# Optimization experiments

Hardware: AMD Instinct MI355X
Metric: run time of the kernel (lower is better)

## Reference

```python
import jax, jax.numpy as jnp
import numpy as np

N_NODES = 100000


def gcn_conv(x, edge_index, W, b):
    # PyG GCNConv: add self-loops, symmetric normalization D^-1/2 (A+I) D^-1/2, transform, aggregate, bias.
    src, dst = edge_index[0], edge_index[1]
    n = x.shape[0]
    xw = x @ W  # [N, out] transform before propagate (PyG order)
    # degree with self-loops (count edges by target + 1)
    deg = jax.ops.segment_sum(jnp.ones_like(dst, dtype=xw.dtype), dst, num_segments=n) + 1.0
    dinv = jax.lax.rsqrt(deg)  # deg >= 1, safe
    norm = dinv[src] * dinv[dst]  # [E]
    msgs = xw[src] * norm[:, None]  # [E, out] gathered, normalized messages
    agg = jax.ops.segment_sum(msgs, dst, num_segments=n)
    # self-loop contribution: norm_ii = dinv_i^2 = 1/deg_i
    agg = agg + xw * (dinv * dinv)[:, None]
    return agg + b


def setup_inputs() -> dict:
    key = jax.random.key(0)
    ks = jax.random.split(key, 8)
    in_c, h1, h2, out_c = 128, 71, 82, 1
    x = jax.random.normal(ks[0], (N_NODES, in_c), dtype=jnp.float32)
    edge_index = jax.random.randint(ks[1], (2, 1600000), 0, N_NODES, dtype=jnp.int64)
    def glorot(k, fan_in, fan_out):
        s = jnp.sqrt(6.0 / (fan_in + fan_out))
        return jax.random.uniform(k, (fan_in, fan_out), jnp.float32, -s, s)
    return {
        "x": x,
        "edge_index": edge_index,
        "W1": glorot(ks[2], in_c, h1), "b1": jnp.zeros((h1,), jnp.float32),
        "W2": glorot(ks[3], h1, h2), "b2": jnp.zeros((h2,), jnp.float32),
        "W3": glorot(ks[4], h2, out_c), "b3": jnp.zeros((out_c,), jnp.float32),
    }


def reference(x, edge_index, W1, b1, W2, b2, W3, b3):
    h = jax.nn.relu(gcn_conv(x, edge_index, W1, b1))
    h = gcn_conv(h, edge_index, W2, b2)  # note: no relu after conv2 in source
    return gcn_conv(h, edge_index, W3, b3)
```

## Files before the change

### kernel.cpp

```cpp
#include <hip/hip_runtime.h>
#include <hip/hip_fp16.h>

#define NNODES 100000
#define NB 196
#define BSHIFT 9
#define BMASK 511
#define BCAP 9216
#define WT_LD 136

typedef _Float16 half8 __attribute__((ext_vector_type(8)));
typedef float floatx4 __attribute__((ext_vector_type(4)));

__global__ void binA_kernel(const int* __restrict__ src, const int* __restrict__ dst,
                            int* __restrict__ bcnt, unsigned* __restrict__ bdata, int E) {
    __shared__ int hist[NB];
    __shared__ int gb[NB];
    __shared__ int cur[NB];
    const int BATCH = 4096;
    for (int base = blockIdx.x * BATCH; base < E; base += gridDim.x * BATCH) {
        for (int i = threadIdx.x; i < NB; i += blockDim.x) hist[i] = 0;
        __syncthreads();
        int s[16], d[16];
        int cnt = 0;
        if (base + BATCH <= E) {
#pragma unroll
            for (int q = 0; q < 4; ++q) {
                int4 sv = ((const int4*)(src + base))[q * 256 + threadIdx.x];
                int4 dv = ((const int4*)(dst + base))[q * 256 + threadIdx.x];
                s[cnt] = sv.x; d[cnt] = dv.x; atomicAdd(&hist[dv.x >> BSHIFT], 1); ++cnt;
                s[cnt] = sv.y; d[cnt] = dv.y; atomicAdd(&hist[dv.y >> BSHIFT], 1); ++cnt;
                s[cnt] = sv.z; d[cnt] = dv.z; atomicAdd(&hist[dv.z >> BSHIFT], 1); ++cnt;
                s[cnt] = sv.w; d[cnt] = dv.w; atomicAdd(&hist[dv.w >> BSHIFT], 1); ++cnt;
            }
        } else {
#pragma unroll
            for (int k = 0; k < 16; ++k) {
                int idx = base + k * 256 + threadIdx.x;
                if (idx < E) {
                    s[cnt] = src[idx];
                    d[cnt] = dst[idx];
                    atomicAdd(&hist[d[cnt] >> BSHIFT], 1);
                    ++cnt;
                }
            }
        }
        __syncthreads();
        for (int i = threadIdx.x; i < NB; i += blockDim.x) {
            int c = hist[i];
            gb[i] = (c > 0) ? atomicAdd(&bcnt[i], c) : 0;
            cur[i] = 0;
        }
        __syncthreads();
        for (int k = 0; k < cnt; ++k) {
            int b = d[k] >> BSHIFT;
            int lo = gb[b] + atomicAdd(&cur[b], 1);
            if (lo < BCAP)
                bdata[(size_t)b * BCAP + lo] = ((unsigned)s[k] << BSHIFT) | ((unsigned)d[k] & BMASK);
        }
        __syncthreads();
    }
}

__global__ __launch_bounds__(1024) void prep_kernel(
        const int* __restrict__ bcnt, int* __restrict__ bstart,
        const float* __restrict__ W2, const float* __restrict__ b2,
        const float* __restrict__ W3, float* __restrict__ w23,
        const float* __restrict__ W1, __half* __restrict__ Wt) {
    if (blockIdx.x == 0) {
        __shared__ int sh[NB];
        int t = threadIdx.x;
        if (t < NB) sh[t] = min(bcnt[t], BCAP);
        __syncthreads();
        if (t == 0) {
            int acc = 0;
            for (int i = 0; i < NB; ++i) { int v = sh[i]; sh[i] = acc; acc += v; }
        }
        __syncthreads();
        if (t < NB) bstart[t] = sh[t];
    } else if (blockIdx.x == 1) {
        int k = threadIdx.x;
        if (k < 71) {
            float a = 0.f;
            for (int j = 0; j < 82; ++j) a += W2[k * 82 + j] * W3[j];
            w23[k] = a;
        } else if (k == 71) {
            float a = 0.f;
            for (int j = 0; j < 82; ++j) a += b2[j] * W3[j];
            w23[71] = a;
        }
    } else {
        for (int i = threadIdx.x; i < 80 * WT_LD; i += blockDim.x) {
            int nn = i / WT_LD, k = i - nn * WT_LD;
            float v = (nn < 71 && k < 128) ? W1[k * 71 + nn] : 0.f;
            Wt[i] = __float2half(v);
        }
    }
}

__global__ __launch_bounds__(1024) void binB2_kernel(
        const int* __restrict__ bcnt, const int* __restrict__ bstart,
        const unsigned* __restrict__ bdata,
        int* __restrict__ deg, int* __restrict__ end_off, float* __restrict__ dinv,
        int* __restrict__ csr, int n) {
    __shared__ unsigned edata[BCAP];
    __shared__ int hist[512];
    __shared__ int cur[512];
    __shared__ int wsum[8];
    int b = blockIdx.x;
    int tid = threadIdx.x;
    int cnt = min(bcnt[b], BCAP);
    int base = bstart[b];
    const unsigned* p = bdata + (size_t)b * BCAP;
    if (tid < 512) hist[tid] = 0;
    __syncthreads();
    for (int i = tid; i < cnt; i += 1024) {
        unsigned e = p[i];
        edata[i] = e;
        atomicAdd(&hist[e & BMASK], 1);
    }
    __syncthreads();
    if (tid < 512) {
        int v = hist[tid];
        int lane = tid & 63;
        int incl = v;
#pragma unroll
        for (int off = 1; off < 64; off <<= 1) {
            int t = __shfl_up(incl, off);
            if (lane >= off) incl += t;
        }
        cur[tid] = incl;
        if (lane == 63) wsum[tid >> 6] = incl;
    }
    __syncthreads();
    if (tid == 0) {
        int acc = 0;
#pragma unroll
        for (int w = 0; w < 8; ++w) { int t = wsum[w]; wsum[w] = acc; acc += t; }
    }
    __syncthreads();
    if (tid < 512) {
        int v = hist[tid];
        int start = base + wsum[tid >> 6] + cur[tid] - v;
        int node = (b << BSHIFT) + tid;
        if (node < n) {
            deg[node] = v;
            end_off[node] = start + v;
            dinv[node] = rsqrtf((float)v + 1.0f);
        }
        cur[tid] = start;
    }
    __syncthreads();
    for (int i = tid; i < cnt; i += 1024) {
        unsigned e = edata[i];
        int pos = atomicAdd(&cur[e & BMASK], 1);
        csr[pos] = (int)(e >> BSHIFT);
    }
}

__global__ __launch_bounds__(256) void xform_mfma(
        const float* __restrict__ x, const __half* __restrict__ Wt,
        const float* __restrict__ scale, __half* __restrict__ msgA,
        __half* __restrict__ msgB, int n) {
    __shared__ __half Wsh[80 * WT_LD];
    {
        const uint4* sp = (const uint4*)Wt;
        uint4* dp = (uint4*)Wsh;
        for (int i = threadIdx.x; i < (80 * WT_LD * 2) / 16; i += blockDim.x) dp[i] = sp[i];
    }
    __syncthreads();
    int lane = threadIdx.x & 63;
    int m = lane & 15, q = lane >> 4;
    int gw = (blockIdx.x * blockDim.x + threadIdx.x) >> 6;
    int nw = (gridDim.x * blockDim.x) >> 6;
    int nrt = n >> 4;
    for (int rt = gw; rt < nrt; rt += nw) {
        int rb = rt << 4;
        const float* xr = x + (size_t)(rb + m) * 128 + q * 8;
        floatx4 acc[5];
#pragma unroll
        for (int t = 0; t < 5; ++t) acc[t] = (floatx4){0.f, 0.f, 0.f, 0.f};
#pragma unroll
        for (int ks = 0; ks < 4; ++ks) {
            float4 f0 = *(const float4*)(xr + ks * 32);
            float4 f1 = *(const float4*)(xr + ks * 32 + 4);
            half8 a;
            a[0] = (_Float16)f0.x; a[1] = (_Float16)f0.y;
            a[2] = (_Float16)f0.z; a[3] = (_Float16)f0.w;
            a[4] = (_Float16)f1.x; a[5] = (_Float16)f1.y;
            a[6] = (_Float16)f1.z; a[7] = (_Float16)f1.w;
#pragma unroll
            for (int t = 0; t < 5; ++t) {
                half8 b = *(const half8*)&Wsh[(t * 16 + m) * WT_LD + ks * 32 + q * 8];
                acc[t] = __builtin_amdgcn_mfma_f32_16x16x32_f16(a, b, acc[t], 0, 0, 0);
            }
        }
        float sc[4];
#pragma unroll
        for (int r = 0; r < 4; ++r) sc[r] = scale[rb + q * 4 + r];
#pragma unroll
        for (int t = 0; t < 5; ++t) {
            int col = t * 16 + m;
#pragma unroll
            for (int r = 0; r < 4; ++r) {
                __half hv = __float2half(acc[t][r] * sc[r]);
                int row = rb + q * 4 + r;
                if (t < 4) {
                    msgA[(size_t)row * 64 + col] = hv;
                } else if (m < 8) {
                    msgB[(size_t)row * 8 + m] = hv;
                }
            }
        }
    }
}

__global__ __launch_bounds__(256) void gather_fused(
        const __half2* __restrict__ msgA, const __half2* __restrict__ msgB,
        const int* __restrict__ csr, const int* __restrict__ end_off,
        const int* __restrict__ deg, const float* __restrict__ dinv,
        const float* __restrict__ b, const float* __restrict__ w23,
        float* __restrict__ g2, int n) {
    int lane = threadIdx.x & 63;
    int wid = (blockIdx.x * blockDim.x + threadIdx.x) >> 6;
    int nwaves = (gridDim.x * blockDim.x) >> 6;
    int k = lane & 31;
    int c = k << 1;
    float bxA = b[c], byA = b[c + 1];
    float w0A = w23[c], w1A = w23[c + 1];
    int p = lane & 3;
    int cb = 64 + (p << 1);
    float bxB = b[cb];
    float byB = (cb + 1 < 71) ? b[cb + 1] : 0.f;
    float w0B = w23[cb];
    float w1B = (cb + 1 < 71) ? w23[cb + 1] : 0.f;
    const char* mA = (const char*)msgA;
    const char* mB = (const char*)msgB;
    unsigned laneOffA = (unsigned)(k << 2);
    unsigned laneOffB = (unsigned)(p << 2);
    for (int node = wid; node < n; node += nwaves) {
        int end = end_off[node];
        int cnt = deg[node];
        int start = end - cnt;
        float ax0 = 0.f, ay0 = 0.f, ax1 = 0.f, ay1 = 0.f;
        float ax2 = 0.f, ay2 = 0.f, ax3 = 0.f, ay3 = 0.f;
        float bxs = 0.f, bys = 0.f;
        for (int base = 0; base < cnt; base += 64) {
            int rem = min(cnt - base, 64);
            int se = (lane < rem) ? csr[start + base + lane] : 0;
            int j = 0;
            for (; j + 7 < rem; j += 8) {
                int sa0 = __builtin_amdgcn_readlane(se, j + 0);
                int sb0 = __builtin_amdgcn_readlane(se, j + 1);
                int sa1 = __builtin_amdgcn_readlane(se, j + 2);
                int sb1 = __builtin_amdgcn_readlane(se, j + 3);
                int sa2 = __builtin_amdgcn_readlane(se, j + 4);
                int sb2 = __builtin_amdgcn_readlane(se, j + 5);
                int sa3 = __builtin_amdgcn_readlane(se, j + 6);
                int sb3 = __builtin_amdgcn_readlane(se, j + 7);
                int s0 = (lane < 32) ? sa0 : sb0;
                int s1 = (lane < 32) ? sa1 : sb1;
                int s2 = (lane < 32) ? sa2 : sb2;
                int s3 = (lane < 32) ? sa3 : sb3;
                float2 v0 = __half22float2(*(const __half2*)(mA + (((unsigned)s0 << 7) | laneOffA)));
                float2 v1 = __half22float2(*(const __half2*)(mA + (((unsigned)s1 << 7) | laneOffA)));
                float2 v2 = __half22float2(*(const __half2*)(mA + (((unsigned)s2 << 7) | laneOffA)));
                float2 v3 = __half22float2(*(const __half2*)(mA + (((unsigned)s3 << 7) | laneOffA)));
                ax0 += v0.x; ay0 += v0.y;  ax1 += v1.x; ay1 += v1.y;
                ax2 += v2.x; ay2 += v2.y;  ax3 += v3.x; ay3 += v3.y;
            }
            for (; j + 1 < rem; j += 2) {
                int sa = __builtin_amdgcn_readlane(se, j);
                int sb = __builtin_amdgcn_readlane(se, j + 1);
                int s = (lane < 32) ? sa : sb;
                float2 v = __half22float2(*(const __half2*)(mA + (((unsigned)s << 7) | laneOffA)));
                ax0 += v.x; ay0 += v.y;
            }
            if (j < rem) {
                int s = __builtin_amdgcn_readlane(se, j);
                float2 v = __half22float2(*(const __half2*)(mA + (((unsigned)s << 7) | laneOffA)));
                if (lane < 32) { ax0 += v.x; ay0 += v.y; }
            }
            for (int t = 0; t < rem; t += 16) {
                int idx = t + (lane >> 2);
                int ss = __shfl(se, (idx < rem) ? idx : (rem - 1));
                float2 v = __half22float2(*(const __half2*)(mB + (((unsigned)ss << 4) | laneOffB)));
                if (idx < rem) { bxs += v.x; bys += v.y; }
            }
        }
        float axA = (ax0 + ax1) + (ax2 + ax3);
        float ayA = (ay0 + ay1) + (ay2 + ay3);
        axA += __shfl_xor(axA, 32);
        ayA += __shfl_xor(ayA, 32);
        {
            float2 sv = __half22float2(msgA[(size_t)node * 32 + k]);
            axA += sv.x; ayA += sv.y;
        }
        bxs += __shfl_xor(bxs, 4);  bxs += __shfl_xor(bxs, 8);
        bxs += __shfl_xor(bxs, 16); bxs += __shfl_xor(bxs, 32);
        bys += __shfl_xor(bys, 4);  bys += __shfl_xor(bys, 8);
        bys += __shfl_xor(bys, 16); bys += __shfl_xor(bys, 32);
        {
            float2 sv = __half22float2(msgB[(size_t)node * 4 + p]);
            bxs += sv.x; bys += sv.y;
        }
        float dv = dinv[node];
        float pa = fmaxf(dv * axA + bxA, 0.f) * w0A + fmaxf(dv * ayA + byA, 0.f) * w1A;
        float pb = fmaxf(dv * bxs + bxB, 0.f) * w0B + fmaxf(dv * bys + byB, 0.f) * w1B;
        float r = ((lane < 32) ? pa : 0.f) + ((lane < 4) ? pb : 0.f);
#pragma unroll
        for (int off = 32; off > 0; off >>= 1) r += __shfl_down(r, off);
        if (lane == 0) g2[node] = dv * r;
    }
}

__global__ void sgather_q(const float* __restrict__ g2, const int* __restrict__ csr,
                          const int* __restrict__ end_off, const int* __restrict__ deg,
                          const float* __restrict__ dinv, const float* __restrict__ w23,
                          float* __restrict__ q, int n) {
    float bw = w23[71];
    int lane = threadIdx.x & 63;
    int g = lane >> 4, k = lane & 15;
    int wid = (blockIdx.x * blockDim.x + threadIdx.x) >> 6;
    int nw = (gridDim.x * blockDim.x) >> 6;
    for (int i0 = wid * 4; i0 < n; i0 += nw * 4) {
        int i = i0 + g;
        float acc = 0.f;
        float dv = 0.f;
        if (i < n) {
            int end = end_off[i];
            int cnt = deg[i];
            int start = end - cnt;
            dv = dinv[i];
            for (int e = k; e < cnt; e += 16) acc += g2[csr[start + e]];
        }
        acc += __shfl_down(acc, 8, 16);
        acc += __shfl_down(acc, 4, 16);
        acc += __shfl_down(acc, 2, 16);
        acc += __shfl_down(acc, 1, 16);
        if (i < n && k == 0) q[i] = dv * (dv * (acc + g2[i]) + bw);
    }
}

__global__ void sgather_out(const float* __restrict__ q, const int* __restrict__ csr,
                            const int* __restrict__ end_off, const int* __restrict__ deg,
                            const float* __restrict__ dinv, const float* __restrict__ b3,
                            float* __restrict__ out, int n) {
    float bv = b3[0];
    int lane = threadIdx.x & 63;
    int g = lane >> 4, k = lane & 15;
    int wid = (blockIdx.x * blockDim.x + threadIdx.x) >> 6;
    int nw = (gridDim.x * blockDim.x) >> 6;
    for (int i0 = wid * 4; i0 < n; i0 += nw * 4) {
        int i = i0 + g;
        float acc = 0.f;
        float dv = 0.f;
        if (i < n) {
            int end = end_off[i];
            int cnt = deg[i];
            int start = end - cnt;
            dv = dinv[i];
            for (int e = k; e < cnt; e += 16) acc += q[csr[start + e]];
        }
        acc += __shfl_down(acc, 8, 16);
        acc += __shfl_down(acc, 4, 16);
        acc += __shfl_down(acc, 2, 16);
        acc += __shfl_down(acc, 1, 16);
        if (i < n && k == 0) out[i] = dv * (acc + q[i]) + bv;
    }
}

extern "C" void kernel_launch(void* const* d_in, const int* in_sizes, int n_in,
                              void* d_out, int out_size, void* d_ws, size_t ws_size,
                              hipStream_t stream) {
    const float* x  = (const float*)d_in[0];
    const int*   ei = (const int*)d_in[1];
    const float* W1 = (const float*)d_in[2];
    const float* b1 = (const float*)d_in[3];
    const float* W2 = (const float*)d_in[4];
    const float* b2 = (const float*)d_in[5];
    const float* W3 = (const float*)d_in[6];
    const float* b3 = (const float*)d_in[7];
    float* out = (float*)d_out;

    const int n = NNODES;
    const int E = in_sizes[1] / 2;
    const int* src = ei;
    const int* dst = ei + E;

    float* ws     = (float*)d_ws;
    float* dinv   = ws;
    int*   deg_i  = (int*)(ws + n);
    int*   offs   = deg_i + n;
    int*   bcnt   = offs + n;
    int*   bstart = bcnt + 256;
    float* w23    = (float*)(bstart + 256);
    __half* Wt    = (__half*)(w23 + 80);
    float* g2     = (float*)(Wt + 11008);
    float* q      = g2 + n;
    int*   csr    = (int*)(q + n);
    __half* msgA  = (__half*)(csr + E + 16);
    __half* msgB  = msgA + (size_t)n * 64;
    unsigned* bdata = (unsigned*)(msgB + (size_t)n * 8);

    hipMemsetAsync(bcnt, 0, 256 * sizeof(int), stream);
    binA_kernel<<<(E + 4095) / 4096, 256, 0, stream>>>(src, dst, bcnt, bdata, E);
    prep_kernel<<<3, 1024, 0, stream>>>(bcnt, bstart, W2, b2, W3, w23, W1, Wt);
    binB2_kernel<<<NB, 1024, 0, stream>>>(bcnt, bstart, bdata, deg_i, offs, dinv, csr, n);

    xform_mfma<<<1563, 256, 0, stream>>>(x, Wt, dinv, msgA, msgB, n);

    gather_fused<<<2048, 256, 0, stream>>>((const __half2*)msgA, (const __half2*)msgB,
                                           csr, offs, deg_i, dinv, b1, w23, g2, n);

    sgather_q<<<1024, 256, 0, stream>>>(g2, csr, offs, deg_i, dinv, w23, q, n);
    sgather_out<<<1024, 256, 0, stream>>>(q, csr, offs, deg_i, dinv, b3, out, n);
}
```

Measured before the change: 238.9 us.

## Gather eight nodes per wavefront with 16-byte half8 row loads

Restructures the first-layer gather so each wavefront handles a tile of 8 nodes, 8 lanes per node. Each lane loads a 16-byte half8 slice of the 64-wide message row plus one half of the tail columns, replacing the one-node-per-wave scheme with 4-byte loads and readlane broadcasts. CSR indices are prefetched two steps ahead, and the self-loop is folded into the loop as an extra iteration. The aim is better memory-level parallelism and fewer idle lanes on low-degree nodes. In exchange, all 8 nodes in a tile iterate to the tile's maximum degree, which leaves lanes idle when degrees vary.

```diff
diff --git a/kernel.cpp b/kernel.cpp
--- a/kernel.cpp
+++ b/kernel.cpp
@@ -215,101 +215,82 @@
 }
 
 __global__ __launch_bounds__(256) void gather_fused(
-        const __half2* __restrict__ msgA, const __half2* __restrict__ msgB,
+        const __half* __restrict__ msgA, const __half* __restrict__ msgB,
         const int* __restrict__ csr, const int* __restrict__ end_off,
         const int* __restrict__ deg, const float* __restrict__ dinv,
         const float* __restrict__ b, const float* __restrict__ w23,
         float* __restrict__ g2, int n) {
     int lane = threadIdx.x & 63;
+    int li = lane & 7;
     int wid = (blockIdx.x * blockDim.x + threadIdx.x) >> 6;
     int nwaves = (gridDim.x * blockDim.x) >> 6;
-    int k = lane & 31;
-    int c = k << 1;
-    float bxA = b[c], byA = b[c + 1];
-    float w0A = w23[c], w1A = w23[c + 1];
-    int p = lane & 3;
-    int cb = 64 + (p << 1);
-    float bxB = b[cb];
-    float byB = (cb + 1 < 71) ? b[cb + 1] : 0.f;
-    float w0B = w23[cb];
-    float w1B = (cb + 1 < 71) ? w23[cb + 1] : 0.f;
+    float bA[8], wA[8];
+#pragma unroll
+    for (int j = 0; j < 8; ++j) { bA[j] = b[8 * li + j]; wA[j] = w23[8 * li + j]; }
+    float bB = (li < 7) ? b[64 + li] : 0.f;
+    float wB = (li < 7) ? w23[64 + li] : 0.f;
     const char* mA = (const char*)msgA;
     const char* mB = (const char*)msgB;
-    unsigned laneOffA = (unsigned)(k << 2);
-    unsigned laneOffB = (unsigned)(p << 2);
-    for (int node = wid; node < n; node += nwaves) {
-        int end = end_off[node];
-        int cnt = deg[node];
-        int start = end - cnt;
-        float ax0 = 0.f, ay0 = 0.f, ax1 = 0.f, ay1 = 0.f;
-        float ax2 = 0.f, ay2 = 0.f, ax3 = 0.f, ay3 = 0.f;
-        float bxs = 0.f, bys = 0.f;
-        for (int base = 0; base < cnt; base += 64) {
-            int rem = min(cnt - base, 64);
-            int se = (lane < rem) ? csr[start + base + lane] : 0;
-            int j = 0;
-            for (; j + 7 < rem; j += 8) {
-                int sa0 = __builtin_amdgcn_readlane(se, j + 0);
-                int sb0 = __builtin_amdgcn_readlane(se, j + 1);
-                int sa1 = __builtin_amdgcn_readlane(se, j + 2);
-                int sb1 = __builtin_amdgcn_readlane(se, j + 3);
-                int sa2 = __builtin_amdgcn_readlane(se, j + 4);
-                int sb2 = __builtin_amdgcn_readlane(se, j + 5);
-                int sa3 = __builtin_amdgcn_readlane(se, j + 6);
-                int sb3 = __builtin_amdgcn_readlane(se, j + 7);
-                int s0 = (lane < 32) ? sa0 : sb0;
-                int s1 = (lane < 32) ? sa1 : sb1;
-                int s2 = (lane < 32) ? sa2 : sb2;
-                int s3 = (lane < 32) ? sa3 : sb3;
-                float2 v0 = __half22float2(*(const __half2*)(mA + (((unsigned)s0 << 7) | laneOffA)));
-                float2 v1 = __half22float2(*(const __half2*)(mA + (((unsigned)s1 << 7) | laneOffA)));
-                float2 v2 = __half22float2(*(const __half2*)(mA + (((unsigned)s2 << 7) | laneOffA)));
-                float2 v3 = __half22float2(*(const __half2*)(mA + (((unsigned)s3 << 7) | laneOffA)));
-                ax0 += v0.x; ay0 += v0.y;  ax1 += v1.x; ay1 += v1.y;
-                ax2 += v2.x; ay2 += v2.y;  ax3 += v3.x; ay3 += v3.y;
-            }
-            for (; j + 1 < rem; j += 2) {
-                int sa = __builtin_amdgcn_readlane(se, j);
-                int sb = __builtin_amdgcn_readlane(se, j + 1);
-                int s = (lane < 32) ? sa : sb;
-                float2 v = __half22float2(*(const __half2*)(mA + (((unsigned)s << 7) | laneOffA)));
-                ax0 += v.x; ay0 += v.y;
-            }
-            if (j < rem) {
-                int s = __builtin_amdgcn_readlane(se, j);
-                float2 v = __half22float2(*(const __half2*)(mA + (((unsigned)s << 7) | laneOffA)));
-                if (lane < 32) { ax0 += v.x; ay0 += v.y; }
-            }
-            for (int t = 0; t < rem; t += 16) {
-                int idx = t + (lane >> 2);
-                int ss = __shfl(se, (idx < rem) ? idx : (rem - 1));
-                float2 v = __half22float2(*(const __half2*)(mB + (((unsigned)ss << 4) | laneOffB)));
-                if (idx < rem) { bxs += v.x; bys += v.y; }
-            }
-        }
-        float axA = (ax0 + ax1) + (ax2 + ax3);
-        float ayA = (ay0 + ay1) + (ay2 + ay3);
-        axA += __shfl_xor(axA, 32);
-        ayA += __shfl_xor(ayA, 32);
-        {
-            float2 sv = __half22float2(msgA[(size_t)node * 32 + k]);
-            axA += sv.x; ayA += sv.y;
-        }
-        bxs += __shfl_xor(bxs, 4);  bxs += __shfl_xor(bxs, 8);
-        bxs += __shfl_xor(bxs, 16); bxs += __shfl_xor(bxs, 32);
-        bys += __shfl_xor(bys, 4);  bys += __shfl_xor(bys, 8);
-        bys += __shfl_xor(bys, 16); bys += __shfl_xor(bys, 32);
-        {
-            float2 sv = __half22float2(msgB[(size_t)node * 4 + p]);
-            bxs += sv.x; bys += sv.y;
-        }
-        float dv = dinv[node];
-        float pa = fmaxf(dv * axA + bxA, 0.f) * w0A + fmaxf(dv * ayA + byA, 0.f) * w1A;
-        float pb = fmaxf(dv * bxs + bxB, 0.f) * w0B + fmaxf(dv * bys + byB, 0.f) * w1B;
-        float r = ((lane < 32) ? pa : 0.f) + ((lane < 4) ? pb : 0.f);
-#pragma unroll
-        for (int off = 32; off > 0; off >>= 1) r += __shfl_down(r, off);
-        if (lane == 0) g2[node] = dv * r;
+    unsigned laneA   = (unsigned)(li << 4);
+    unsigned laneBof = (unsigned)((li >> 1) << 2);
+    unsigned laneBsh = (unsigned)((li & 1) << 4);
+    int ntiles = (n + 7) >> 3;
+    for (int tile = wid; tile < ntiles; tile += nwaves) {
+        int node = (tile << 3) + (lane >> 3);
+        int d = -1, st = 0; float dv = 0.f;
+        if (node < n) {
+            int e = end_off[node];
+            d = deg[node];
+            st = e - d;
+            dv = dinv[node];
+        }
+        int tmax = d;
+        tmax = max(tmax, __shfl_xor(tmax, 8));
+        tmax = max(tmax, __shfl_xor(tmax, 16));
+        tmax = max(tmax, __shfl_xor(tmax, 32));
+        tmax = __builtin_amdgcn_readfirstlane(tmax);
+        float acc[8];
+#pragma unroll
+        for (int j = 0; j < 8; ++j) acc[j] = 0.f;
+        float bsum = 0.f;
+        int c0 = csr[(0 < d) ? st : 0];
+        int c1 = csr[(1 < d) ? st + 1 : 0];
+        for (int i = 0; i <= tmax; i += 2) {
+            int p0 = csr[(i + 2 < d) ? st + i + 2 : 0];
+            int p1 = csr[(i + 3 < d) ? st + i + 3 : 0];
+            if (i <= d) {
+                unsigned idx = (unsigned)((i < d) ? c0 : node);
+                half8 row = *(const half8*)(mA + ((idx << 7) | laneA));
+                unsigned bw = *(const unsigned*)(mB + ((idx << 4) | laneBof));
+#pragma unroll
+                for (int j = 0; j < 8; ++j) acc[j] += (float)row[j];
+                unsigned short us = (unsigned short)(bw >> laneBsh);
+                _Float16 hf;
+                __builtin_memcpy(&hf, &us, 2);
+                bsum += (float)hf;
+            }
+            if (i + 1 <= d) {
+                unsigned idx = (unsigned)((i + 1 < d) ? c1 : node);
+                half8 row = *(const half8*)(mA + ((idx << 7) | laneA));
+                unsigned bw = *(const unsigned*)(mB + ((idx << 4) | laneBof));
+#pragma unroll
+                for (int j = 0; j < 8; ++j) acc[j] += (float)row[j];
+                unsigned short us = (unsigned short)(bw >> laneBsh);
+                _Float16 hf;
+                __builtin_memcpy(&hf, &us, 2);
+                bsum += (float)hf;
+            }
+            c0 = p0;
+            c1 = p1;
+        }
+        float p = 0.f;
+#pragma unroll
+        for (int j = 0; j < 8; ++j) p += fmaxf(dv * acc[j] + bA[j], 0.f) * wA[j];
+        p += fmaxf(dv * bsum + bB, 0.f) * wB;
+        p += __shfl_xor(p, 1);
+        p += __shfl_xor(p, 2);
+        p += __shfl_xor(p, 4);
+        if (node < n && li == 0) g2[node] = dv * p;
     }
 }
 
@@ -409,8 +390,7 @@
 
     xform_mfma<<<1563, 256, 0, stream>>>(x, Wt, dinv, msgA, msgB, n);
 
-    gather_fused<<<2048, 256, 0, stream>>>((const __half2*)msgA, (const __half2*)msgB,
-                                           csr, offs, deg_i, dinv, b1, w23, g2, n);
+    gather_fused<<<1563, 256, 0, stream>>>(msgA, msgB, csr, offs, deg_i, dinv, b1, w23, g2, n);
 
     sgather_q<<<1024, 256, 0, stream>>>(g2, csr, offs, deg_i, dinv, w23, q, n);
     sgather_out<<<1024, 256, 0, stream>>>(q, csr, offs, deg_i, dinv, b3, out, n);
```

After: 225.7 us. 5.5% less time.
